# Optimization experiments

Measured on AMD Instinct MI355X. Metric: run time of the kernel, lower is better.

Reference implementation:

```python
import jax, jax.numpy as jnp
import numpy as np

D = 1024       # d_model
DR = 1024      # d_rec
FFN = 4096     # ffn_inner
K = 4          # conv_kernel
B, T = 2, 4096
CHUNK = 64
EPS = 1e-6


def setup_inputs() -> dict:
    key = jax.random.key(0)
    ks = jax.random.split(key, 8)
    s = lambda k, shape, scale: jax.random.normal(k, shape, jnp.float32) * scale
    db = np.zeros((DR,), np.float32)
    q = DR // 4
    db[:q] = -2.2
    db[q:3 * q] = 0.0
    db[3 * q:] = 4.6
    return {
        "x": s(ks[0], (B, T, D), 1.0),
        "pre_norm_w": jnp.ones((D,), jnp.float32),
        "conv_w": s(ks[1], (D, 1, K), 0.3),
        "conv_b": jnp.zeros((D,), jnp.float32),
        "w_a": s(ks[2], (DR, D), 0.02),
        "w_i": s(ks[3], (DR, D), 0.02),
        "w_v": s(ks[4], (DR, D), 0.02),
        "out_proj_w": s(ks[5], (D, DR), 0.02),
        "decay_bias": jnp.asarray(db),
        "ffn_norm_w": jnp.ones((D,), jnp.float32),
        "w_gate_up": s(ks[6], (2 * FFN, D), 0.02),
        "w_down": s(ks[7], (D, FFN), 0.02),
    }


def rmsnorm(x, w):
    return x * jax.lax.rsqrt(jnp.mean(x * x, axis=-1, keepdims=True) + EPS) * w


def lin(x, w):  # nn.Linear weight layout (out, in)
    return jnp.einsum('btd,od->bto', x, w)


def causal_conv(h, w, b):
    # depthwise causal conv: h (B,T,D), w (D,1,K)
    hc = jnp.transpose(h, (0, 2, 1))  # (B,D,T)
    out = jax.lax.conv_general_dilated(
        hc, w, window_strides=(1,), padding=[(K - 1, 0)],
        dimension_numbers=('NCH', 'OIH', 'NCH'), feature_group_count=D)
    return jnp.transpose(out, (0, 2, 1)) + b


def chunked_scan(a, v):
    b, s, d = a.shape
    pad = (-s) % CHUNK
    af = jnp.pad(a, ((0, 0), (0, pad), (0, 0)), constant_values=1.0)
    vf = jnp.pad(v, ((0, 0), (0, pad), (0, 0)))
    n = (s + pad) // CHUNK
    dc = af.reshape(b, n, CHUNK, d)
    vc = vf.reshape(b, n, CHUNK, d)
    cum_decay = jnp.exp(jnp.cumsum(jnp.log(jnp.clip(dc, 1e-10)), axis=2))
    intra = cum_decay * jnp.cumsum(vc / jnp.clip(cum_decay, 1e-10), axis=2)

    def step(state, xs):
        cd, it = xs  # (B,CHUNK,d) each
        cs = it + cd * state[:, None, :]
        return cs[:, -1], cs

    _, states = jax.lax.scan(
        step, jnp.zeros((b, d), jnp.float32),
        (jnp.transpose(cum_decay, (1, 0, 2, 3)), jnp.transpose(intra, (1, 0, 2, 3))))
    return jnp.transpose(states, (1, 0, 2, 3)).reshape(b, n * CHUNK, d)[:, :s]


def reference(x, pre_norm_w, conv_w, conv_b, w_a, w_i, w_v, out_proj_w,
              decay_bias, ffn_norm_w, w_gate_up, w_down):
    h = rmsnorm(x, pre_norm_w)
    h = causal_conv(h, conv_w, conv_b)
    a = jax.nn.sigmoid(lin(h, w_a) + decay_bias)
    i_gate = jax.nn.sigmoid(lin(h, w_i))
    v = lin(h, w_v)
    input_signal = jnp.sqrt(jnp.clip(1.0 - a * a, 1e-8)) * (i_gate * v)
    rec_out = chunked_scan(a, input_signal).astype(x.dtype)
    x = x + lin(rec_out, out_proj_w)
    hn = rmsnorm(x, ffn_norm_w)
    gu = lin(hn, w_gate_up)
    gate, up = gu[..., :FFN], gu[..., FFN:]
    x = x + lin(jax.nn.silu(gate) * up, w_down)
    return x
```

## Files before the change

### kernel.cpp

```cpp
#include <hip/hip_runtime.h>

typedef __bf16 bf16_t;
typedef bf16_t bf16x4 __attribute__((ext_vector_type(4)));
typedef bf16_t bf16x8 __attribute__((ext_vector_type(8)));
typedef float f32x4 __attribute__((ext_vector_type(4)));

#define DD 1024
#define TT 4096

__device__ __forceinline__ void gload16(const void* g, void* l) {
    __builtin_amdgcn_global_load_lds(
        (const __attribute__((address_space(1))) void*)g,
        (__attribute__((address_space(3))) void*)l, 16, 0, 0);
}

__global__ __launch_bounds__(256) void cvt_bf16_k(const float* __restrict__ s,
                                                  bf16_t* __restrict__ d, int n) {
    int i = (blockIdx.x * 256 + threadIdx.x) * 4;
    if (i < n) {
        const float4 v = *(const float4*)(s + i);
        bf16x4 o;
        o[0] = (bf16_t)v.x; o[1] = (bf16_t)v.y; o[2] = (bf16_t)v.z; o[3] = (bf16_t)v.w;
        *(bf16x4*)(d + i) = o;
    }
}

__global__ __launch_bounds__(256) void cvt_ileave_k(const float* __restrict__ s0,
                                                    const float* __restrict__ s1,
                                                    bf16_t* __restrict__ d, int total) {
    int i = (blockIdx.x * 256 + threadIdx.x) * 4;
    if (i < total) {
        const int rp = i >> 10, k = i & 1023;
        const int c = rp >> 1;
        const float* src = ((rp & 1) ? s1 : s0) + (long)c * 1024 + k;
        const float4 v = *(const float4*)src;
        bf16x4 o;
        o[0] = (bf16_t)v.x; o[1] = (bf16_t)v.y; o[2] = (bf16_t)v.z; o[3] = (bf16_t)v.w;
        *(bf16x4*)(d + i) = o;
    }
}

__global__ __launch_bounds__(256) void rmsnorm_k(const float* __restrict__ x,
                                                 const float* __restrict__ w,
                                                 bf16_t* __restrict__ ob) {
    const long row = blockIdx.x;
    const float* xr = x + row * DD;
    const int t4 = threadIdx.x * 4;
    float4 v = *(const float4*)(xr + t4);
    float s = v.x*v.x + v.y*v.y + v.z*v.z + v.w*v.w;
    #pragma unroll
    for (int off = 1; off < 64; off <<= 1) s += __shfl_xor(s, off);
    __shared__ float red[4];
    if ((threadIdx.x & 63) == 0) red[threadIdx.x >> 6] = s;
    __syncthreads();
    float tot = red[0] + red[1] + red[2] + red[3];
    float sc = rsqrtf(tot * (1.0f / DD) + 1e-6f);
    float4 wv = *(const float4*)(w + t4);
    bf16x4 o;
    o[0] = (bf16_t)(v.x*sc*wv.x); o[1] = (bf16_t)(v.y*sc*wv.y);
    o[2] = (bf16_t)(v.z*sc*wv.z); o[3] = (bf16_t)(v.w*sc*wv.w);
    *(bf16x4*)(ob + row * DD + t4) = o;
}

__global__ __launch_bounds__(256) void conv_k(const bf16_t* __restrict__ h,
                                              const float* __restrict__ cw,
                                              const float* __restrict__ cb,
                                              bf16_t* __restrict__ hc) {
    const long idx = (long)blockIdx.x * 256 + threadIdx.x;
    const int d = (int)(idx & (DD - 1));
    const long bt = idx >> 10;
    const int t = (int)(bt & (TT - 1));
    const float w0 = cw[d*4+0], w1 = cw[d*4+1], w2 = cw[d*4+2], w3 = cw[d*4+3];
    const bf16_t* hp = h + bt * DD + d;
    float acc = cb[d] + (float)hp[0] * w3;
    if (t >= 1) acc += (float)hp[-DD]     * w2;
    if (t >= 2) acc += (float)hp[-2*DD]   * w1;
    if (t >= 3) acc += (float)hp[-3*DD]   * w0;
    hc[idx] = (bf16_t)acc;
}

__global__ __launch_bounds__(256) void scan1_k(const float* __restrict__ ap,
                                               const float* __restrict__ sp,
                                               float* __restrict__ cd63,
                                               float* __restrict__ i63) {
    const int d = blockIdx.x * 256 + threadIdx.x;
    const int c = blockIdx.y;
    const int b = blockIdx.z;
    const long rowbase = (long)b * TT + (long)c * 64;
    float la = 0.0f, rs = 0.0f, cdv = 0.0f, it = 0.0f;
    for (int t = 0; t < 64; t++) {
        const long off = (rowbase + t) * DD + d;
        const float a = ap[off];
        const float s = sp[off];
        const float sig = sqrtf(fmaxf(1.0f - a * a, 1e-8f)) * s;
        la += __logf(fmaxf(a, 1e-10f));
        cdv = __expf(la);
        rs += sig / fmaxf(cdv, 1e-10f);
        it = cdv * rs;
    }
    const long o = ((long)b * 64 + c) * DD + d;
    cd63[o] = cdv;
    i63[o]  = it;
}

__global__ __launch_bounds__(256) void scan2_k(const float* __restrict__ cd63,
                                               const float* __restrict__ i63,
                                               float* __restrict__ carry_in) {
    const int g = blockIdx.x * 256 + threadIdx.x;
    const int b = g >> 10, d = g & (DD - 1);
    float st = 0.0f;
    for (int c = 0; c < 64; c++) {
        const long o = ((long)b * 64 + c) * DD + d;
        carry_in[o] = st;
        st = i63[o] + cd63[o] * st;
    }
}

__global__ __launch_bounds__(256) void scan3_k(const float* __restrict__ ap,
                                               const float* __restrict__ sp,
                                               const float* __restrict__ carry_in,
                                               bf16_t* __restrict__ rec) {
    const int d = blockIdx.x * 256 + threadIdx.x;
    const int c = blockIdx.y;
    const int b = blockIdx.z;
    const long rowbase = (long)b * TT + (long)c * 64;
    const float carry = carry_in[((long)b * 64 + c) * DD + d];
    float la = 0.0f, rs = 0.0f;
    for (int t = 0; t < 64; t++) {
        const long off = (rowbase + t) * DD + d;
        const float a = ap[off];
        const float s = sp[off];
        const float sig = sqrtf(fmaxf(1.0f - a * a, 1e-8f)) * s;
        la += __logf(fmaxf(a, 1e-10f));
        const float cdv = __expf(la);
        rs += sig / fmaxf(cdv, 1e-10f);
        rec[off] = (bf16_t)(cdv * rs + cdv * carry);
    }
}

enum { EPI_SIGB = 0, EPI_ADDRES = 1, EPI_IV = 2, EPI_GU = 3 };

template<int EPI, int NREP>
__global__ __launch_bounds__(512, 2) void gemm2p_k(const bf16_t* __restrict__ Ag,
                                                   const bf16_t* __restrict__ Bg,
                                                   int M, int N, int K,
                                                   float* outF, bf16_t* outB,
                                                   const float* aux, int ldc) {
    constexpr int BN  = NREP * 64;
    constexpr int ASZ = 16384;
    constexpr int BSZ = BN * 64;
    constexpr int BUF = ASZ + BSZ;
    extern __shared__ bf16_t smem[];
    const int tid = threadIdx.x;
    const int l = tid & 63;
    const int w = tid >> 6;
    const int wm = w >> 2, wn = w & 3;

    const int gx = gridDim.x;
    const int gy = gridDim.y;
    const int lin = blockIdx.y * gx + blockIdx.x;
    long row0, col0;
    if ((gy & 7) == 0) {
        const int rpc = gy >> 3;
        const int q = lin >> 3;
        row0 = (long)((lin & 7) * rpc + q % rpc) * 256;
        col0 = (long)(q / rpc) * (long)BN;
    } else {
        row0 = (long)blockIdx.y * 256;
        col0 = (long)blockIdx.x * BN;
    }

    const int srow = l >> 3;
    const int scol = ((l & 7) ^ srow) * 8;
    const long aBase = row0 + srow;
    const long bBase = col0 + srow;
    const int R0a = w * 32;
    const int R0b = w * (BN / 8);

    const int NT = K >> 6;
    f32x4 acc[8][NREP] = {};

    const int lq2 = (l >> 4) * 16;
    const int rA = wm * 128 + (l & 15);
    const int rB = wn * (NREP * 16) + (l & 15);
    const int eA0 = rA * 64 + ((lq2 ^ ((rA & 7) << 4)) >> 1);
    const int eB0 = ASZ + rB * 64 + ((lq2 ^ ((rB & 7) << 4)) >> 1);

    #define STAGE_A(tt, off)                                                          \
        { const long kgk = (long)(tt) * 64 + scol;                                    \
          _Pragma("unroll")                                                           \
          for (int i = 0; i < 4; i++)                                                 \
              gload16(Ag + (aBase + R0a + i * 8) * (long)K + kgk,                     \
                      &smem[(off) + (R0a + i * 8) * 64]); }
    #define STAGE_B(tt, off)                                                          \
        { const long kgk = (long)(tt) * 64 + scol;                                    \
          _Pragma("unroll")                                                           \
          for (int i = 0; i < NREP; i++)                                              \
              gload16(Bg + (bBase + R0b + i * 8) * (long)K + kgk,                     \
                      &smem[(off) + ASZ + (R0b + i * 8) * 64]); }

    STAGE_A(0, 0); STAGE_B(0, 0);
    STAGE_A(1, BUF); STAGE_B(1, BUF);
    if constexpr (NREP == 4) { asm volatile("s_waitcnt vmcnt(8)" ::: "memory"); }
    else                     { asm volatile("s_waitcnt vmcnt(6)" ::: "memory"); }
    asm volatile("s_barrier" ::: "memory");

    bf16x8 pA[2][4], pB[2][NREP];
    #pragma unroll
    for (int kk = 0; kk < 2; kk++) {
        const int xo = kk * 32;
        #pragma unroll
        for (int n = 0; n < NREP; n++)
            pB[kk][n] = *(const bf16x8*)&smem[(eB0 ^ xo) + n * 1024];
        #pragma unroll
        for (int m = 0; m < 4; m++)
            pA[kk][m] = *(const bf16x8*)&smem[(eA0 ^ xo) + m * 1024];
    }

    for (int t = 0; t < NT; t++) {
        const int co = (t & 1) ? BUF : 0;
        const int oo = BUF - co;
        bf16x8 a1[2][4];

        __builtin_amdgcn_s_setprio(1);
        #pragma unroll
        for (int kk = 0; kk < 2; kk++)
            #pragma unroll
            for (int m = 0; m < 4; m++)
                #pragma unroll
                for (int n = 0; n < NREP; n++)
                    acc[m][n] = __builtin_amdgcn_mfma_f32_16x16x32_bf16(pA[kk][m], pB[kk][n], acc[m][n], 0, 0, 0);
        __builtin_amdgcn_s_setprio(0);
        #pragma unroll
        for (int kk = 0; kk < 2; kk++) {
            const int xo = kk * 32;
            #pragma unroll
            for (int m = 0; m < 4; m++)
                a1[kk][m] = *(const bf16x8*)&smem[co + (eA0 ^ xo) + 4096 + m * 1024];
        }
        asm volatile("s_barrier" ::: "memory");

        if (t + 2 < NT) { STAGE_A(t + 2, co); STAGE_B(t + 2, co); }
        __builtin_amdgcn_s_setprio(1);
        #pragma unroll
        for (int kk = 0; kk < 2; kk++)
            #pragma unroll
            for (int m = 0; m < 4; m++)
                #pragma unroll
                for (int n = 0; n < NREP; n++)
                    acc[m + 4][n] = __builtin_amdgcn_mfma_f32_16x16x32_bf16(a1[kk][m], pB[kk][n], acc[m + 4][n], 0, 0, 0);
        __builtin_amdgcn_s_setprio(0);
        if (t + 2 < NT) {
            if constexpr (NREP == 4) { asm volatile("s_waitcnt vmcnt(8)" ::: "memory"); }
            else                     { asm volatile("s_waitcnt vmcnt(6)" ::: "memory"); }
        } else if (t + 1 < NT) {
            asm volatile("s_waitcnt vmcnt(0)" ::: "memory");
        }
        asm volatile("s_barrier" ::: "memory");
        if (t + 1 < NT) {
            #pragma unroll
            for (int kk = 0; kk < 2; kk++) {
                const int xo = kk * 32;
                #pragma unroll
                for (int n = 0; n < NREP; n++)
                    pB[kk][n] = *(const bf16x8*)&smem[oo + (eB0 ^ xo) + n * 1024];
                #pragma unroll
                for (int m = 0; m < 4; m++)
                    pA[kk][m] = *(const bf16x8*)&smem[oo + (eA0 ^ xo) + m * 1024];
            }
        }
    }
    #undef STAGE_A
    #undef STAGE_B

    #pragma unroll
    for (int m = 0; m < 8; m++) {
        const long r0 = row0 + wm * 128 + m * 16 + (l >> 4) * 4;
        #pragma unroll
        for (int n = 0; n < NREP; n++) {
            const long cc = col0 + wn * (NREP * 16) + n * 16 + (l & 15);
            f32x4 v = acc[m][n];
            #pragma unroll
            for (int j = 0; j < 4; j++) {
                const long r = r0 + j;
                const float xv = v[j];
                if (EPI == EPI_SIGB) {
                    outF[r * ldc + cc] = 1.0f / (1.0f + __expf(-(xv + aux[cc])));
                } else if (EPI == EPI_ADDRES) {
                    outF[r * ldc + cc] = xv + aux[r * ldc + cc];
                } else if (EPI == EPI_IV) {
                    const float px = __shfl_xor(xv, 1);
                    if ((l & 1) == 0)
                        outF[r * ldc + (cc >> 1)] = px / (1.0f + __expf(-xv));
                } else {
                    const float px = __shfl_xor(xv, 1);
                    if ((l & 1) == 0)
                        outB[r * ldc + (cc >> 1)] = (bf16_t)(xv / (1.0f + __expf(-xv)) * px);
                }
            }
        }
    }
}

extern "C" void kernel_launch(void* const* d_in, const int* in_sizes, int n_in,
                              void* d_out, int out_size, void* d_ws, size_t ws_size,
                              hipStream_t stream) {
    const float* x   = (const float*)d_in[0];
    const float* pnw = (const float*)d_in[1];
    const float* cw  = (const float*)d_in[2];
    const float* cb  = (const float*)d_in[3];
    const float* wa  = (const float*)d_in[4];
    const float* wi  = (const float*)d_in[5];
    const float* wv  = (const float*)d_in[6];
    const float* wop = (const float*)d_in[7];
    const float* db  = (const float*)d_in[8];
    const float* fnw = (const float*)d_in[9];
    const float* wgu = (const float*)d_in[10];
    const float* wdn = (const float*)d_in[11];
    float* out = (float*)d_out;

    char* ws = (char*)d_ws;
    bf16_t* wab   = (bf16_t*)(ws + 0);
    bf16_t* wivb  = (bf16_t*)(ws + 2097152);
    bf16_t* wopb  = (bf16_t*)(ws + 6291456);
    bf16_t* wgub  = (bf16_t*)(ws + 8388608);
    bf16_t* wdnb  = (bf16_t*)(ws + 25165824);
    bf16_t* hb    = (bf16_t*)(ws + 33554432);
    bf16_t* hn    = hb;
    bf16_t* hc    = (bf16_t*)(ws + 50331648);
    bf16_t* rec   = hc;
    float*  a_p   = (float*)(ws + 67108864);
    float*  s_p   = (float*)(ws + 100663296);
    bf16_t* act   = (bf16_t*)(ws + 67108864);
    float*  cd63  = (float*)(ws + 134217728);
    float*  i63   = (float*)(ws + 134742016);
    float*  carry = (float*)(ws + 135266304);

    const int LDS4 = 131072;
    const int LDS2 = 98304;
    hipFuncSetAttribute((const void*)gemm2p_k<EPI_SIGB, 2>,   hipFuncAttributeMaxDynamicSharedMemorySize, LDS2);
    hipFuncSetAttribute((const void*)gemm2p_k<EPI_IV, 4>,     hipFuncAttributeMaxDynamicSharedMemorySize, LDS4);
    hipFuncSetAttribute((const void*)gemm2p_k<EPI_ADDRES, 2>, hipFuncAttributeMaxDynamicSharedMemorySize, LDS2);
    hipFuncSetAttribute((const void*)gemm2p_k<EPI_GU, 4>,     hipFuncAttributeMaxDynamicSharedMemorySize, LDS4);

    cvt_bf16_k  <<<1024, 256, 0, stream>>>(wa,  wab,  1048576);
    cvt_ileave_k<<<2048, 256, 0, stream>>>(wi,  wv, wivb, 2097152);
    cvt_bf16_k  <<<1024, 256, 0, stream>>>(wop, wopb, 1048576);
    cvt_ileave_k<<<8192, 256, 0, stream>>>(wgu, wgu + 4194304, wgub, 8388608);
    cvt_bf16_k  <<<4096, 256, 0, stream>>>(wdn, wdnb, 4194304);

    rmsnorm_k<<<8192, 256, 0, stream>>>(x, pnw, hb);
    conv_k<<<32768, 256, 0, stream>>>(hb, cw, cb, hc);

    gemm2p_k<EPI_SIGB, 2><<<dim3(8, 32), 512, LDS2, stream>>>(hc, wab,  8192, 1024, 1024,
                                                              a_p, nullptr, db, 1024);
    gemm2p_k<EPI_IV, 4>  <<<dim3(8, 32), 512, LDS4, stream>>>(hc, wivb, 8192, 2048, 1024,
                                                              s_p, nullptr, nullptr, 1024);
    scan1_k<<<dim3(4, 64, 2), 256, 0, stream>>>(a_p, s_p, cd63, i63);
    scan2_k<<<8, 256, 0, stream>>>(cd63, i63, carry);
    scan3_k<<<dim3(4, 64, 2), 256, 0, stream>>>(a_p, s_p, carry, rec);

    gemm2p_k<EPI_ADDRES, 2><<<dim3(8, 32), 512, LDS2, stream>>>(rec, wopb, 8192, 1024, 1024,
                                                                out, nullptr, x, 1024);
    rmsnorm_k<<<8192, 256, 0, stream>>>(out, fnw, hn);
    gemm2p_k<EPI_GU, 4><<<dim3(32, 32), 512, LDS4, stream>>>(hn, wgub, 8192, 8192, 1024,
                                                             nullptr, act, nullptr, 4096);
    gemm2p_k<EPI_ADDRES, 2><<<dim3(8, 32), 512, LDS2, stream>>>(act, wdnb, 8192, 1024, 4096,
                                                                out, nullptr, out, 1024);
}
```

Before: 468.8 us.

## Restructure GEMM main loop into four barrier-separated phases with staggered A/B prefetch

The bf16 GEMM K-loop is rewritten from a two-phase schedule into four phases, one per k-half and row-half. Each phase loads its fragments from LDS, issues a slice of the next tile's global-to-LDS copies, then runs one MFMA block. The A tile is now prefetched one step ahead while B stays two steps ahead, so the global loads are spread evenly across the iteration instead of issued in one burst. This adds more s_barriers per iteration and shortens the lookahead for A, which may expose more memory latency or sync overhead.

```diff
diff --git a/kernel.cpp b/kernel.cpp
--- a/kernel.cpp
+++ b/kernel.cpp
@@ -141,7 +141,7 @@
 enum { EPI_SIGB = 0, EPI_ADDRES = 1, EPI_IV = 2, EPI_GU = 3 };
 
 template<int EPI, int NREP>
-__global__ __launch_bounds__(512, 2) void gemm2p_k(const bf16_t* __restrict__ Ag,
+__global__ __launch_bounds__(512, 2) void gemm4p_k(const bf16_t* __restrict__ Ag,
                                                    const bf16_t* __restrict__ Bg,
                                                    int M, int N, int K,
                                                    float* outF, bf16_t* outB,
@@ -186,92 +186,100 @@
     const int eA0 = rA * 64 + ((lq2 ^ ((rA & 7) << 4)) >> 1);
     const int eB0 = ASZ + rB * 64 + ((lq2 ^ ((rB & 7) << 4)) >> 1);
 
-    #define STAGE_A(tt, off)                                                          \
-        { const long kgk = (long)(tt) * 64 + scol;                                    \
-          _Pragma("unroll")                                                           \
-          for (int i = 0; i < 4; i++)                                                 \
-              gload16(Ag + (aBase + R0a + i * 8) * (long)K + kgk,                     \
-                      &smem[(off) + (R0a + i * 8) * 64]); }
-    #define STAGE_B(tt, off)                                                          \
-        { const long kgk = (long)(tt) * 64 + scol;                                    \
-          _Pragma("unroll")                                                           \
-          for (int i = 0; i < NREP; i++)                                              \
-              gload16(Bg + (bBase + R0b + i * 8) * (long)K + kgk,                     \
-                      &smem[(off) + ASZ + (R0b + i * 8) * 64]); }
-
-    STAGE_A(0, 0); STAGE_B(0, 0);
-    STAGE_A(1, BUF); STAGE_B(1, BUF);
-    if constexpr (NREP == 4) { asm volatile("s_waitcnt vmcnt(8)" ::: "memory"); }
-    else                     { asm volatile("s_waitcnt vmcnt(6)" ::: "memory"); }
-    asm volatile("s_barrier" ::: "memory");
-
-    bf16x8 pA[2][4], pB[2][NREP];
-    #pragma unroll
-    for (int kk = 0; kk < 2; kk++) {
-        const int xo = kk * 32;
+    #define ST_A(tt, off, i)                                                        \
+        gload16(Ag + (aBase + R0a + (i) * 8) * (long)K + (long)(tt) * 64 + scol,    \
+                &smem[(off) + (R0a + (i) * 8) * 64])
+    #define ST_B(tt, off, i)                                                        \
+        gload16(Bg + (bBase + R0b + (i) * 8) * (long)K + (long)(tt) * 64 + scol,    \
+                &smem[(off) + ASZ + (R0b + (i) * 8) * 64])
+    #define BAR asm volatile("s_barrier" ::: "memory")
+
+    #pragma unroll
+    for (int i = 0; i < NREP; i++) ST_B(0, 0, i);
+    #pragma unroll
+    for (int i = 0; i < 4; i++)    ST_A(0, 0, i);
+    #pragma unroll
+    for (int i = 0; i < NREP; i++) ST_B(1, BUF, i);
+    if constexpr (NREP == 4) { asm volatile("s_waitcnt vmcnt(4)" ::: "memory"); }
+    else                     { asm volatile("s_waitcnt vmcnt(2)" ::: "memory"); }
+    BAR;
+
+    for (int t = 0; t < NT; t++) {
+        const int cur = (t & 1) * BUF;
+        const int oth = BUF - cur;
+        bf16x8 bk0[NREP], bk1[NREP], af[4];
+
         #pragma unroll
         for (int n = 0; n < NREP; n++)
-            pB[kk][n] = *(const bf16x8*)&smem[(eB0 ^ xo) + n * 1024];
-        #pragma unroll
-        for (int m = 0; m < 4; m++)
-            pA[kk][m] = *(const bf16x8*)&smem[(eA0 ^ xo) + m * 1024];
-    }
-
-    for (int t = 0; t < NT; t++) {
-        const int co = (t & 1) ? BUF : 0;
-        const int oo = BUF - co;
-        bf16x8 a1[2][4];
-
+            bk0[n] = *(const bf16x8*)&smem[cur + eB0 + n * 1024];
+        #pragma unroll
+        for (int m = 0; m < 4; m++)
+            af[m] = *(const bf16x8*)&smem[cur + eA0 + m * 1024];
+        if (t + 1 < NT) { ST_A(t + 1, oth, 0); ST_A(t + 1, oth, 1); }
+        BAR;
         __builtin_amdgcn_s_setprio(1);
         #pragma unroll
-        for (int kk = 0; kk < 2; kk++)
-            #pragma unroll
-            for (int m = 0; m < 4; m++)
-                #pragma unroll
-                for (int n = 0; n < NREP; n++)
-                    acc[m][n] = __builtin_amdgcn_mfma_f32_16x16x32_bf16(pA[kk][m], pB[kk][n], acc[m][n], 0, 0, 0);
+        for (int m = 0; m < 4; m++)
+            #pragma unroll
+            for (int n = 0; n < NREP; n++)
+                acc[m][n] = __builtin_amdgcn_mfma_f32_16x16x32_bf16(af[m], bk0[n], acc[m][n], 0, 0, 0);
         __builtin_amdgcn_s_setprio(0);
-        #pragma unroll
-        for (int kk = 0; kk < 2; kk++) {
-            const int xo = kk * 32;
-            #pragma unroll
-            for (int m = 0; m < 4; m++)
-                a1[kk][m] = *(const bf16x8*)&smem[co + (eA0 ^ xo) + 4096 + m * 1024];
-        }
-        asm volatile("s_barrier" ::: "memory");
-
-        if (t + 2 < NT) { STAGE_A(t + 2, co); STAGE_B(t + 2, co); }
+        BAR;
+
+        #pragma unroll
+        for (int n = 0; n < NREP; n++)
+            bk1[n] = *(const bf16x8*)&smem[cur + (eB0 ^ 32) + n * 1024];
+        #pragma unroll
+        for (int m = 0; m < 4; m++)
+            af[m] = *(const bf16x8*)&smem[cur + (eA0 ^ 32) + m * 1024];
+        if (t + 1 < NT) { ST_A(t + 1, oth, 2); ST_A(t + 1, oth, 3); }
+        BAR;
         __builtin_amdgcn_s_setprio(1);
         #pragma unroll
-        for (int kk = 0; kk < 2; kk++)
-            #pragma unroll
-            for (int m = 0; m < 4; m++)
-                #pragma unroll
-                for (int n = 0; n < NREP; n++)
-                    acc[m + 4][n] = __builtin_amdgcn_mfma_f32_16x16x32_bf16(a1[kk][m], pB[kk][n], acc[m + 4][n], 0, 0, 0);
+        for (int m = 0; m < 4; m++)
+            #pragma unroll
+            for (int n = 0; n < NREP; n++)
+                acc[m][n] = __builtin_amdgcn_mfma_f32_16x16x32_bf16(af[m], bk1[n], acc[m][n], 0, 0, 0);
         __builtin_amdgcn_s_setprio(0);
+        BAR;
+
+        #pragma unroll
+        for (int m = 0; m < 4; m++)
+            af[m] = *(const bf16x8*)&smem[cur + eA0 + 4096 + m * 1024];
+        if (t + 2 < NT) { ST_B(t + 2, cur, 0); ST_B(t + 2, cur, 1); }
+        BAR;
+        __builtin_amdgcn_s_setprio(1);
+        #pragma unroll
+        for (int m = 0; m < 4; m++)
+            #pragma unroll
+            for (int n = 0; n < NREP; n++)
+                acc[m + 4][n] = __builtin_amdgcn_mfma_f32_16x16x32_bf16(af[m], bk0[n], acc[m + 4][n], 0, 0, 0);
+        __builtin_amdgcn_s_setprio(0);
+        BAR;
+
+        #pragma unroll
+        for (int m = 0; m < 4; m++)
+            af[m] = *(const bf16x8*)&smem[cur + (eA0 ^ 32) + 4096 + m * 1024];
         if (t + 2 < NT) {
-            if constexpr (NREP == 4) { asm volatile("s_waitcnt vmcnt(8)" ::: "memory"); }
-            else                     { asm volatile("s_waitcnt vmcnt(6)" ::: "memory"); }
-        } else if (t + 1 < NT) {
+            if constexpr (NREP == 4) { ST_B(t + 2, cur, 2); ST_B(t + 2, cur, 3); }
+            if constexpr (NREP == 4) { asm volatile("s_waitcnt vmcnt(4)" ::: "memory"); }
+            else                     { asm volatile("s_waitcnt vmcnt(2)" ::: "memory"); }
+        } else {
             asm volatile("s_waitcnt vmcnt(0)" ::: "memory");
         }
-        asm volatile("s_barrier" ::: "memory");
-        if (t + 1 < NT) {
-            #pragma unroll
-            for (int kk = 0; kk < 2; kk++) {
-                const int xo = kk * 32;
-                #pragma unroll
-                for (int n = 0; n < NREP; n++)
-                    pB[kk][n] = *(const bf16x8*)&smem[oo + (eB0 ^ xo) + n * 1024];
-                #pragma unroll
-                for (int m = 0; m < 4; m++)
-                    pA[kk][m] = *(const bf16x8*)&smem[oo + (eA0 ^ xo) + m * 1024];
-            }
-        }
-    }
-    #undef STAGE_A
-    #undef STAGE_B
+        BAR;
+        __builtin_amdgcn_s_setprio(1);
+        #pragma unroll
+        for (int m = 0; m < 4; m++)
+            #pragma unroll
+            for (int n = 0; n < NREP; n++)
+                acc[m + 4][n] = __builtin_amdgcn_mfma_f32_16x16x32_bf16(af[m], bk1[n], acc[m + 4][n], 0, 0, 0);
+        __builtin_amdgcn_s_setprio(0);
+        BAR;
+    }
+    #undef ST_A
+    #undef ST_B
+    #undef BAR
 
     #pragma unroll
     for (int m = 0; m < 8; m++) {
@@ -338,10 +346,10 @@
 
     const int LDS4 = 131072;
     const int LDS2 = 98304;
-    hipFuncSetAttribute((const void*)gemm2p_k<EPI_SIGB, 2>,   hipFuncAttributeMaxDynamicSharedMemorySize, LDS2);
-    hipFuncSetAttribute((const void*)gemm2p_k<EPI_IV, 4>,     hipFuncAttributeMaxDynamicSharedMemorySize, LDS4);
-    hipFuncSetAttribute((const void*)gemm2p_k<EPI_ADDRES, 2>, hipFuncAttributeMaxDynamicSharedMemorySize, LDS2);
-    hipFuncSetAttribute((const void*)gemm2p_k<EPI_GU, 4>,     hipFuncAttributeMaxDynamicSharedMemorySize, LDS4);
+    hipFuncSetAttribute((const void*)gemm4p_k<EPI_SIGB, 2>,   hipFuncAttributeMaxDynamicSharedMemorySize, LDS2);
+    hipFuncSetAttribute((const void*)gemm4p_k<EPI_IV, 4>,     hipFuncAttributeMaxDynamicSharedMemorySize, LDS4);
+    hipFuncSetAttribute((const void*)gemm4p_k<EPI_ADDRES, 2>, hipFuncAttributeMaxDynamicSharedMemorySize, LDS2);
+    hipFuncSetAttribute((const void*)gemm4p_k<EPI_GU, 4>,     hipFuncAttributeMaxDynamicSharedMemorySize, LDS4);
 
     cvt_bf16_k  <<<1024, 256, 0, stream>>>(wa,  wab,  1048576);
     cvt_ileave_k<<<2048, 256, 0, stream>>>(wi,  wv, wivb, 2097152);
@@ -352,19 +360,19 @@
     rmsnorm_k<<<8192, 256, 0, stream>>>(x, pnw, hb);
     conv_k<<<32768, 256, 0, stream>>>(hb, cw, cb, hc);
 
-    gemm2p_k<EPI_SIGB, 2><<<dim3(8, 32), 512, LDS2, stream>>>(hc, wab,  8192, 1024, 1024,
+    gemm4p_k<EPI_SIGB, 2><<<dim3(8, 32), 512, LDS2, stream>>>(hc, wab,  8192, 1024, 1024,
                                                               a_p, nullptr, db, 1024);
-    gemm2p_k<EPI_IV, 4>  <<<dim3(8, 32), 512, LDS4, stream>>>(hc, wivb, 8192, 2048, 1024,
+    gemm4p_k<EPI_IV, 4>  <<<dim3(8, 32), 512, LDS4, stream>>>(hc, wivb, 8192, 2048, 1024,
                                                               s_p, nullptr, nullptr, 1024);
     scan1_k<<<dim3(4, 64, 2), 256, 0, stream>>>(a_p, s_p, cd63, i63);
     scan2_k<<<8, 256, 0, stream>>>(cd63, i63, carry);
     scan3_k<<<dim3(4, 64, 2), 256, 0, stream>>>(a_p, s_p, carry, rec);
 
-    gemm2p_k<EPI_ADDRES, 2><<<dim3(8, 32), 512, LDS2, stream>>>(rec, wopb, 8192, 1024, 1024,
+    gemm4p_k<EPI_ADDRES, 2><<<dim3(8, 32), 512, LDS2, stream>>>(rec, wopb, 8192, 1024, 1024,
                                                                 out, nullptr, x, 1024);
     rmsnorm_k<<<8192, 256, 0, stream>>>(out, fnw, hn);
-    gemm2p_k<EPI_GU, 4><<<dim3(32, 32), 512, LDS4, stream>>>(hn, wgub, 8192, 8192, 1024,
+    gemm4p_k<EPI_GU, 4><<<dim3(32, 32), 512, LDS4, stream>>>(hn, wgub, 8192, 8192, 1024,
                                                              nullptr, act, nullptr, 4096);
-    gemm2p_k<EPI_ADDRES, 2><<<dim3(8, 32), 512, LDS2, stream>>>(act, wdnb, 8192, 1024, 4096,
+    gemm4p_k<EPI_ADDRES, 2><<<dim3(8, 32), 512, LDS2, stream>>>(act, wdnb, 8192, 1024, 4096,
                                                                 out, nullptr, out, 1024);
 }
```

Result: slower. 478.3 us (+2.0%).
